# Optimization experiments

Measured on AMD Instinct MI355X. Metric: run time of the kernel, lower is better.

Reference implementation:

```python
import jax, jax.numpy as jnp
import numpy as np

BETA = 0.95
THRESHOLD = 1.0
SLOPE = 25.0
NUM_STEPS = 25

@jax.custom_vjp
def spike_fn(x):
    # Heaviside forward, fast-sigmoid surrogate backward (snntorch surrogate.fast_sigmoid(slope=25))
    return (x > 0).astype(x.dtype)

def _spike_fwd(x):
    return spike_fn(x), x

def _spike_bwd(x, g):
    return (g / (SLOPE * jnp.abs(x) + 1.0) ** 2,)

spike_fn.defvjp(_spike_fwd, _spike_bwd)

def _leaky_step(mem, cur):
    # snntorch Leaky, reset_mechanism='subtract', threshold=1.0:
    # reset computed from PREVIOUS mem, detached
    reset = jax.lax.stop_gradient(spike_fn(mem - THRESHOLD))
    mem = BETA * mem + cur - reset * THRESHOLD
    spk = spike_fn(mem - THRESHOLD)
    return spk, mem

def setup_inputs() -> dict:
    key = jax.random.key(0)
    ks = jax.random.split(key, 7)
    B, D, H = 65536, 64, 1024
    s = lambda k, shp, fan: jax.random.normal(k, shp, jnp.float32) * (1.0 / np.sqrt(fan))
    return {
        'x':  jax.random.normal(ks[0], (B, D), jnp.float32),
        'W1': s(ks[1], (D, H), D),
        'b1': s(ks[2], (H,), D),
        'W2': s(ks[3], (H, H // 2), H),
        'b2': s(ks[4], (H // 2,), H),
        'W3': s(ks[5], (H // 2, 1), H // 2),
        'b3': s(ks[6], (1,), H // 2),
    }

def reference(x, W1, b1, W2, b2, W3, b3):
    B = x.shape[0]
    cur1 = x @ W1 + b1  # constant across time steps (input is static)
    mem1 = jnp.zeros((B, W1.shape[1]), x.dtype)
    mem2 = jnp.zeros((B, W2.shape[1]), x.dtype)
    mem3 = jnp.zeros((B, W3.shape[1]), x.dtype)

    def step(carry, _):
        mem1, mem2, mem3 = carry
        spk1, mem1 = _leaky_step(mem1, cur1)
        cur2 = spk1 @ W2 + b2
        spk2, mem2 = _leaky_step(mem2, cur2)
        cur3 = spk2 @ W3 + b3
        spk3, mem3 = _leaky_step(mem3, cur3)
        return (mem1, mem2, mem3), mem3

    _, mem_rec = jax.lax.scan(step, (mem1, mem2, mem3), None, length=NUM_STEPS)
    # mem_rec: [num_steps, B, 1]
    return jax.nn.sigmoid(jnp.mean(mem_rec, axis=0))
```

## Files before the change

### kernel.cpp

```cpp
#include <hip/hip_runtime.h>

typedef unsigned int u32;
typedef unsigned long long u64;
typedef float f32x4 __attribute__((ext_vector_type(4)));

__device__ __forceinline__ float leaky(float m, float cur) {
  float r = (m > 1.0f) ? 1.0f : 0.0f;
  return __fsub_rn(__fadd_rn(__fmul_rn(0.95f, m), cur), r);
}

__global__ __launch_bounds__(256) void k_spk1(
    const float* __restrict__ x, const float* __restrict__ W1,
    const float* __restrict__ b1, u32* __restrict__ masks,
    int s0, int Sc) {
  __shared__ float w1s[8 * 1024];
  const int tid = threadIdx.x, lane = tid & 63, w = tid >> 6;
  const int sl = blockIdx.x * 4 + w;
  const size_t s = (size_t)s0 + sl;

  float c1[16];
#pragma unroll
  for (int j = 0; j < 16; ++j) c1[j] = 0.0f;
#pragma unroll 1
  for (int ch = 0; ch < 8; ++ch) {
    __syncthreads();
#pragma unroll
    for (int it = 0; it < 8; ++it) {
      int v = tid + it * 256;
      *(f32x4*)(w1s + v * 4) =
          *(const f32x4*)(W1 + (size_t)(ch * 8 + (v >> 8)) * 1024 + (v & 255) * 4);
    }
    __syncthreads();
#pragma unroll 1
    for (int dl = 0; dl < 8; ++dl) {
      float xv = x[s * 64 + ch * 8 + dl];
#pragma unroll
      for (int j = 0; j < 16; ++j)
        c1[j] = fmaf(xv, w1s[dl * 1024 + j * 64 + lane], c1[j]);
    }
  }
#pragma unroll
  for (int j = 0; j < 16; ++j) c1[j] = __fadd_rn(c1[j], b1[j * 64 + lane]);

  float m1[16];
#pragma unroll
  for (int j = 0; j < 16; ++j) m1[j] = 0.0f;

#pragma unroll 1
  for (int t = 0; t < 25; ++t) {
#pragma unroll
    for (int j = 0; j < 16; ++j) {
      m1[j] = leaky(m1[j], c1[j]);
      u64 ball = __ballot(m1[j] > 1.0f);
      if (lane == 0) {
        masks[((size_t)t * 32 + 2 * j) * Sc + sl] = (u32)ball;
        masks[((size_t)t * 32 + 2 * j + 1) * Sc + sl] = (u32)(ball >> 32);
      }
    }
  }
}

#define FOR16(M) M(0) M(1) M(2) M(3) M(4) M(5) M(6) M(7) \
                 M(8) M(9) M(10) M(11) M(12) M(13) M(14) M(15)

#define DECL_ACC(i)                                                     \
  float aA##i##_0 = 0.f, aA##i##_1 = 0.f, aA##i##_2 = 0.f, aA##i##_3 = 0.f; \
  float aB##i##_0 = 0.f, aB##i##_1 = 0.f, aB##i##_2 = 0.f, aB##i##_3 = 0.f;

#define LOADW(i) const u32 w##i = (u32)__builtin_amdgcn_readfirstlane((int)mp[i]);

#define E4(A, R, g) A##_0 = fmaf(g, R[0], A##_0); A##_1 = fmaf(g, R[1], A##_1); \
                    A##_2 = fmaf(g, R[2], A##_2); A##_3 = fmaf(g, R[3], A##_3);

#define GFMA_A(i) { const float g = (w##i & mA) ? 1.0f : 0.0f; \
                    E4(aA##i, rA0, g) E4(aB##i, rA1, g) }
#define GFMA_B(i) { const float g = (w##i & mB) ? 1.0f : 0.0f; \
                    E4(aA##i, rB0, g) E4(aB##i, rB1, g) }

#define STORE16(i) {                                                    \
  float* op = cur2 + ((size_t)(sl0 + i) * 25 + t) * 512 + lq;           \
  op[0] = __fadd_rn(aA##i##_0, bv0); op[1] = __fadd_rn(aA##i##_1, bv1); \
  op[2] = __fadd_rn(aA##i##_2, bv2); op[3] = __fadd_rn(aA##i##_3, bv3); \
  op[256] = __fadd_rn(aB##i##_0, bv4); op[257] = __fadd_rn(aB##i##_1, bv5); \
  op[258] = __fadd_rn(aB##i##_2, bv6); op[259] = __fadd_rn(aB##i##_3, bv7); }

__global__ __launch_bounds__(256) void k_cur2(
    const float* __restrict__ W2, const float* __restrict__ b2,
    const u32* __restrict__ masks, float* __restrict__ cur2, int Sc) {
  const int tid = threadIdx.x, lane = tid & 63, w = tid >> 6;
  const int task = blockIdx.x * 4 + w;
  const int grp = task / 25, t = task - grp * 25;
  const int sl0 = grp * 16;
  const int lq = lane * 4;

  FOR16(DECL_ACC)

  const float* wp = W2 + lq;
  f32x4 rA0 = *(const f32x4*)(wp);
  f32x4 rA1 = *(const f32x4*)(wp + 256);
  f32x4 rB0, rB1;

#pragma unroll 1
  for (int kw = 0; kw < 32; ++kw) {
    const u32* mp = masks + ((size_t)t * 32 + kw) * Sc + sl0;
    FOR16(LOADW)
#pragma unroll 1
    for (int k2 = 0; k2 < 32; k2 += 2) {
      const int k = kw * 32 + k2;
      const u32 mA = 1u << k2;
      const u32 mB = 2u << k2;
      const float* pB = wp + (size_t)(k + 1) * 512;
      rB0 = *(const f32x4*)(pB);
      rB1 = *(const f32x4*)(pB + 256);
      FOR16(GFMA_A)
      const int kn = (k + 2 < 1024) ? k + 2 : 1023;
      const float* pA = wp + (size_t)kn * 512;
      rA0 = *(const f32x4*)(pA);
      rA1 = *(const f32x4*)(pA + 256);
      FOR16(GFMA_B)
    }
  }

  const float bv0 = b2[lq], bv1 = b2[lq + 1], bv2 = b2[lq + 2], bv3 = b2[lq + 3];
  const float bv4 = b2[256 + lq], bv5 = b2[257 + lq];
  const float bv6 = b2[258 + lq], bv7 = b2[259 + lq];
  FOR16(STORE16)
}

__global__ __launch_bounds__(256) void k_tail(
    const float* __restrict__ cur2, const float* __restrict__ W3,
    const float* __restrict__ b3, float* __restrict__ out, int s0, int Sc) {
  __shared__ float w3s[512];
  const int tid = threadIdx.x, lane = tid & 63, w = tid >> 6;
  const int sl = blockIdx.x * 4 + w;
  for (int i = tid; i < 512; i += 256) w3s[i] = W3[i];
  __syncthreads();

  float m2[8];
#pragma unroll
  for (int j = 0; j < 8; ++j) m2[j] = 0.0f;
  float m3 = 0.0f;
  double s3 = 0.0;
  const float b3v = b3[0];
  const float* cp = cur2 + (size_t)sl * 25 * 512;

#pragma unroll 1
  for (int t = 0; t < 25; ++t) {
    u64 s2b[8];
#pragma unroll
    for (int j = 0; j < 8; ++j) {
      float cur = cp[t * 512 + j * 64 + lane];
      m2[j] = leaky(m2[j], cur);
      s2b[j] = __ballot(m2[j] > 1.0f);
    }
    if (lane == 0) {
      float c3 = 0.0f;
#pragma unroll 1
      for (int j = 0; j < 8; ++j) {
        u64 mm = s2b[j];
        const int nb = j * 64;
        if (mm) {
          int nn = __ffsll(mm) - 1;
          mm &= mm - 1;
          float wv = w3s[nb + nn];
          while (mm) {
            int n2 = __ffsll(mm) - 1;
            mm &= mm - 1;
            float wn = w3s[nb + n2];
            c3 = __fadd_rn(c3, wv);
            wv = wn;
          }
          c3 = __fadd_rn(c3, wv);
        }
      }
      c3 = __fadd_rn(c3, b3v);
      m3 = leaky(m3, c3);
      s3 += (double)m3;
    }
  }
  if (lane == 0) {
    double z = s3 / 25.0;
    out[s0 + sl] = (float)(1.0 / (1.0 + exp(-z)));
  }
}

__global__ __launch_bounds__(256) void k_snn(
    const float* __restrict__ x, const float* __restrict__ W1,
    const float* __restrict__ b1, const float* __restrict__ W2,
    const float* __restrict__ b2, const float* __restrict__ W3,
    const float* __restrict__ b3, float* __restrict__ out) {
  __shared__ float w1s[8 * 1024];
  __shared__ float w3s[512];
  __shared__ u32 spkm[4][32];
  const int tid = threadIdx.x, lane = tid & 63, w = tid >> 6;
  const size_t s = (size_t)blockIdx.x * 4 + w;

  for (int i = tid; i < 512; i += 256) w3s[i] = W3[i];

  float c1[16];
#pragma unroll
  for (int j = 0; j < 16; ++j) c1[j] = 0.0f;
#pragma unroll 1
  for (int ch = 0; ch < 8; ++ch) {
    __syncthreads();
#pragma unroll
    for (int it = 0; it < 8; ++it) {
      int v = tid + it * 256;
      *(f32x4*)(w1s + v * 4) =
          *(const f32x4*)(W1 + (size_t)(ch * 8 + (v >> 8)) * 1024 + (v & 255) * 4);
    }
    __syncthreads();
#pragma unroll 1
    for (int dl = 0; dl < 8; ++dl) {
      float xv = x[s * 64 + ch * 8 + dl];
#pragma unroll
      for (int j = 0; j < 16; ++j)
        c1[j] = fmaf(xv, w1s[dl * 1024 + j * 64 + lane], c1[j]);
    }
  }
#pragma unroll
  for (int j = 0; j < 16; ++j) c1[j] = __fadd_rn(c1[j], b1[j * 64 + lane]);

  float m1[16];
#pragma unroll
  for (int j = 0; j < 16; ++j) m1[j] = 0.0f;
  float m2[8];
#pragma unroll
  for (int j = 0; j < 8; ++j) m2[j] = 0.0f;
  float b2l[8];
#pragma unroll
  for (int j = 0; j < 8; ++j) b2l[j] = b2[j * 64 + lane];
  const float b3v = b3[0];
  float m3 = 0.0f;
  double s3 = 0.0;

#pragma unroll 1
  for (int t = 0; t < 25; ++t) {
#pragma unroll
    for (int j = 0; j < 16; ++j) {
      m1[j] = leaky(m1[j], c1[j]);
      u64 ball = __ballot(m1[j] > 1.0f);
      if (lane == 0) {
        spkm[w][2 * j]     = (u32)ball;
        spkm[w][2 * j + 1] = (u32)(ball >> 32);
      }
    }
    __syncthreads();

    float c2[8];
#pragma unroll
    for (int j = 0; j < 8; ++j) c2[j] = 0.0f;
#pragma unroll 1
    for (int kw = 0; kw < 32; ++kw) {
      u32 mask = spkm[w][kw];
      int kbase = kw * 32;
      while (mask) {
        int kk = __ffs(mask) - 1;
        mask &= mask - 1;
        const float* wr = W2 + (size_t)(kbase + kk) * 512;
#pragma unroll
        for (int j = 0; j < 8; ++j)
          c2[j] = __fadd_rn(c2[j], wr[j * 64 + lane]);
      }
    }
    u64 s2b[8];
#pragma unroll
    for (int j = 0; j < 8; ++j) {
      float cur = __fadd_rn(c2[j], b2l[j]);
      m2[j] = leaky(m2[j], cur);
      s2b[j] = __ballot(m2[j] > 1.0f);
    }

    if (lane == 0) {
      float c3 = 0.0f;
#pragma unroll 1
      for (int j = 0; j < 8; ++j) {
        u64 mm = s2b[j];
        int nb = j * 64;
        while (mm) {
          int nn = __ffsll(mm) - 1;
          mm &= mm - 1;
          c3 = __fadd_rn(c3, w3s[nb + nn]);
        }
      }
      c3 = __fadd_rn(c3, b3v);
      m3 = leaky(m3, c3);
      s3 += (double)m3;
    }
    __syncthreads();
  }

  if (lane == 0) {
    double z = s3 / 25.0;
    out[s] = (float)(1.0 / (1.0 + exp(-z)));
  }
}

extern "C" void kernel_launch(void* const* d_in, const int* in_sizes, int n_in,
                              void* d_out, int out_size, void* d_ws, size_t ws_size,
                              hipStream_t stream) {
  const float* x  = (const float*)d_in[0];
  const float* W1 = (const float*)d_in[1];
  const float* b1 = (const float*)d_in[2];
  const float* W2 = (const float*)d_in[3];
  const float* b2 = (const float*)d_in[4];
  const float* W3 = (const float*)d_in[5];
  const float* b3 = (const float*)d_in[6];
  float* out = (float*)d_out;

  const long long per_sample = 54400;
  long long smax = (d_ws != nullptr) ? (long long)(ws_size / per_sample) : 0;
  long long scap = smax > 65536 ? 65536 : smax;
  int S = (int)(scap & ~63LL);

  if (S >= 256) {
    u32* masks = (u32*)d_ws;
    float* cur2 = (float*)((char*)d_ws + (size_t)S * 3200);
    for (int s0 = 0; s0 < 65536; s0 += S) {
      int Sc = (65536 - s0 < S) ? (65536 - s0) : S;
      hipLaunchKernelGGL(k_spk1, dim3(Sc / 4), dim3(256), 0, stream,
                         x, W1, b1, masks, s0, Sc);
      hipLaunchKernelGGL(k_cur2, dim3(((Sc / 16) * 25) / 4), dim3(256), 0, stream,
                         W2, b2, masks, cur2, Sc);
      hipLaunchKernelGGL(k_tail, dim3(Sc / 4), dim3(256), 0, stream,
                         cur2, W3, b3, out, s0, Sc);
    }
  } else {
    hipLaunchKernelGGL(k_snn, dim3(16384), dim3(256), 0, stream,
                       x, W1, b1, W2, b2, W3, b3, out);
  }
}
```

Baseline: 25.55 ms.

## Stage W2 tiles in double-buffered shared memory for k_cur2

The k_cur2 kernel now loads 16-row tiles of W2 cooperatively into a double-buffered LDS array, prefetching the next tile into registers while the current one is consumed, instead of having every wave stream W2 rows directly from global memory. The four waves in a block share each tile, so global and L2 traffic for W2 drops by about four times. In exchange it adds a block-wide barrier per tile, 64 KB of LDS per block (which limits occupancy), and extra registers for the prefetch staging.

```diff
diff --git a/kernel.cpp b/kernel.cpp
--- a/kernel.cpp
+++ b/kernel.cpp
@@ -62,20 +62,21 @@
 
 #define FOR16(M) M(0) M(1) M(2) M(3) M(4) M(5) M(6) M(7) \
                  M(8) M(9) M(10) M(11) M(12) M(13) M(14) M(15)
+#define FOR16A1(M, a) M(0,a) M(1,a) M(2,a) M(3,a) M(4,a) M(5,a) M(6,a) M(7,a) \
+                      M(8,a) M(9,a) M(10,a) M(11,a) M(12,a) M(13,a) M(14,a) M(15,a)
 
 #define DECL_ACC(i)                                                     \
   float aA##i##_0 = 0.f, aA##i##_1 = 0.f, aA##i##_2 = 0.f, aA##i##_3 = 0.f; \
   float aB##i##_0 = 0.f, aB##i##_1 = 0.f, aB##i##_2 = 0.f, aB##i##_3 = 0.f;
 
-#define LOADW(i) const u32 w##i = (u32)__builtin_amdgcn_readfirstlane((int)mp[i]);
-
-#define E4(A, R, g) A##_0 = fmaf(g, R[0], A##_0); A##_1 = fmaf(g, R[1], A##_1); \
-                    A##_2 = fmaf(g, R[2], A##_2); A##_3 = fmaf(g, R[3], A##_3);
-
-#define GFMA_A(i) { const float g = (w##i & mA) ? 1.0f : 0.0f; \
-                    E4(aA##i, rA0, g) E4(aB##i, rA1, g) }
-#define GFMA_B(i) { const float g = (w##i & mB) ? 1.0f : 0.0f; \
-                    E4(aA##i, rB0, g) E4(aB##i, rB1, g) }
+#define DECL_W(i) u32 w##i;
+#define LOADW(i)  w##i = (u32)__builtin_amdgcn_readfirstlane((int)mp[i]);
+
+#define GSQ(i, MB) { const float g = (w##i & (MB)) ? 1.0f : 0.0f;       \
+  aA##i##_0 = fmaf(g, q0[0], aA##i##_0); aA##i##_1 = fmaf(g, q0[1], aA##i##_1); \
+  aA##i##_2 = fmaf(g, q0[2], aA##i##_2); aA##i##_3 = fmaf(g, q0[3], aA##i##_3); \
+  aB##i##_0 = fmaf(g, q1[0], aB##i##_0); aB##i##_1 = fmaf(g, q1[1], aB##i##_1); \
+  aB##i##_2 = fmaf(g, q1[2], aB##i##_2); aB##i##_3 = fmaf(g, q1[3], aB##i##_3); }
 
 #define STORE16(i) {                                                    \
   float* op = cur2 + ((size_t)(sl0 + i) * 25 + t) * 512 + lq;           \
@@ -87,6 +88,7 @@
 __global__ __launch_bounds__(256) void k_cur2(
     const float* __restrict__ W2, const float* __restrict__ b2,
     const u32* __restrict__ masks, float* __restrict__ cur2, int Sc) {
+  __shared__ float w2s[2][16][512];
   const int tid = threadIdx.x, lane = tid & 63, w = tid >> 6;
   const int task = blockIdx.x * 4 + w;
   const int grp = task / 25, t = task - grp * 25;
@@ -94,31 +96,51 @@
   const int lq = lane * 4;
 
   FOR16(DECL_ACC)
-
-  const float* wp = W2 + lq;
-  f32x4 rA0 = *(const f32x4*)(wp);
-  f32x4 rA1 = *(const f32x4*)(wp + 256);
-  f32x4 rB0, rB1;
-
-#pragma unroll 1
-  for (int kw = 0; kw < 32; ++kw) {
-    const u32* mp = masks + ((size_t)t * 32 + kw) * Sc + sl0;
-    FOR16(LOADW)
-#pragma unroll 1
-    for (int k2 = 0; k2 < 32; k2 += 2) {
-      const int k = kw * 32 + k2;
-      const u32 mA = 1u << k2;
-      const u32 mB = 2u << k2;
-      const float* pB = wp + (size_t)(k + 1) * 512;
-      rB0 = *(const f32x4*)(pB);
-      rB1 = *(const f32x4*)(pB + 256);
-      FOR16(GFMA_A)
-      const int kn = (k + 2 < 1024) ? k + 2 : 1023;
-      const float* pA = wp + (size_t)kn * 512;
-      rA0 = *(const f32x4*)(pA);
-      rA1 = *(const f32x4*)(pA + 256);
-      FOR16(GFMA_B)
-    }
+  FOR16(DECL_W)
+  f32x4 st[8];
+
+  {
+    const float* gsrc = W2 + tid * 4;
+#pragma unroll
+    for (int it = 0; it < 8; ++it) st[it] = *(const f32x4*)(gsrc + it * 1024);
+    float* dst = &w2s[0][0][0] + tid * 4;
+#pragma unroll
+    for (int it = 0; it < 8; ++it) *(f32x4*)(dst + it * 1024) = st[it];
+  }
+  __syncthreads();
+
+#pragma unroll 1
+  for (int tile = 0; tile < 64; ++tile) {
+    const float* cb = (tile & 1) ? &w2s[1][0][0] : &w2s[0][0][0];
+    float* nb = (tile & 1) ? &w2s[0][0][0] : &w2s[1][0][0];
+
+    if (tile < 63) {
+      const float* gsrc = W2 + (size_t)(tile + 1) * 8192 + tid * 4;
+#pragma unroll
+      for (int it = 0; it < 8; ++it) st[it] = *(const f32x4*)(gsrc + it * 1024);
+    }
+
+    const int kw = tile >> 1;
+    if (!(tile & 1)) {
+      const u32* mp = masks + ((size_t)t * 32 + kw) * Sc + sl0;
+      FOR16(LOADW)
+    }
+    const int hb = (tile & 1) * 16;
+
+#pragma unroll
+    for (int r = 0; r < 16; ++r) {
+      const f32x4 q0 = *(const f32x4*)(cb + r * 512 + lq);
+      const f32x4 q1 = *(const f32x4*)(cb + r * 512 + 256 + lq);
+      const u32 mb = 1u << (hb + r);
+      FOR16A1(GSQ, mb)
+    }
+
+    if (tile < 63) {
+      float* dst = nb + tid * 4;
+#pragma unroll
+      for (int it = 0; it < 8; ++it) *(f32x4*)(dst + it * 1024) = st[it];
+    }
+    __syncthreads();
   }
 
   const float bv0 = b2[lq], bv1 = b2[lq + 1], bv2 = b2[lq + 2], bv3 = b2[lq + 3];
```

Result: slower. 43.43 ms (+70.0%).
